# Performance work log

Measured on AMD Instinct MI355X. Metric: run time of the kernel, lower is better.

Reference implementation:

```python
import jax, jax.numpy as jnp
import numpy as np

HEADS = 16

def setup_inputs() -> dict:
    key = jax.random.key(0)
    ks = jax.random.split(key, 5)
    dim = 1024
    x = jax.random.normal(ks[0], (2, 2048, dim), dtype=jnp.float32)
    scale = 1.0 / np.sqrt(dim)
    Wq = jax.random.normal(ks[1], (dim, dim), dtype=jnp.float32) * scale
    Wk = jax.random.normal(ks[2], (dim, dim), dtype=jnp.float32) * scale
    Wv = jax.random.normal(ks[3], (dim, dim), dtype=jnp.float32) * scale
    Wo = jax.random.normal(ks[4], (dim, dim), dtype=jnp.float32) * scale
    return {"x": x, "Wq": Wq, "Wk": Wk, "Wv": Wv, "Wo": Wo}

def reference(x, Wq, Wk, Wv, Wo):
    b, n, dim = x.shape
    h = HEADS
    d = dim // h
    # projections: torch Linear y = x @ W.T (W is [out,in])
    def split_heads(t):
        return t.reshape(b, n, h, d).transpose(0, 2, 1, 3)  # b h n d
    q = split_heads(x @ Wq.T)
    k = split_heads(x @ Wk.T)
    v = split_heads(x @ Wv.T)
    scale = jnp.asarray(d, x.dtype) ** -0.5
    dots = jnp.einsum('bhid,bhjd->bhij', q, k) * scale
    # causal mask: positions j > i masked (triu with diagonal 1 since i == j)
    i_idx = jnp.arange(n)[:, None]
    j_idx = jnp.arange(n)[None, :]
    mask_value = -jnp.finfo(dots.dtype).max
    dots = jnp.where(j_idx > i_idx, mask_value, dots)
    attn = jax.nn.softmax(dots, axis=-1)  # dropout p=0 (eval) is identity
    out = jnp.einsum('bhij,bhjd->bhid', attn, v)
    out = out.transpose(0, 2, 1, 3).reshape(b, n, dim)
    return out @ Wo.T
```

## Files before the change

kernel.cpp:

```cpp
#include <hip/hip_runtime.h>
#include <hip/hip_bf16.h>

#define BATCH 2
#define SEQ   2048
#define DIM   1024
#define HEADS 16
#define DIMH  64
#define BK    32
#define LOG2E 1.44269504088896340736f
#define SM_SHIFT 16.0f

typedef __attribute__((ext_vector_type(8))) short short8;
typedef __attribute__((ext_vector_type(4))) short short4v;
typedef __attribute__((ext_vector_type(4))) float floatx4;

static __device__ __forceinline__ void gload_lds16(const void* g, void* l) {
    __builtin_amdgcn_global_load_lds(
        (const __attribute__((address_space(1))) void*)g,
        (__attribute__((address_space(3))) void*)l, 16, 0, 0);
}

static __device__ __forceinline__ unsigned pk_trunc(float a, float b) {
    return (__float_as_uint(b) & 0xffff0000u) | (__float_as_uint(a) >> 16);
}

__global__ __launch_bounds__(256) void conv_all(
    const float* __restrict__ x,  const float* __restrict__ Wq,
    const float* __restrict__ Wk, const float* __restrict__ Wv,
    const float* __restrict__ Wo,
    __hip_bfloat16* __restrict__ dst, __hip_bfloat16* __restrict__ dwo)
{
    const size_t NX = (size_t)BATCH * SEQ * DIM;
    const size_t NW = (size_t)DIM * DIM;
    size_t i = ((size_t)blockIdx.x * 256 + threadIdx.x) * 4;
    if (i >= NX + 4 * NW) return;
    const float* src; __hip_bfloat16* d;
    if (i < NX) { src = x + i; d = dst + i; }
    else if (i < NX + 3 * NW) {
        size_t j = i - NX;
        int w = (int)(j >> 20);
        src = ((w == 0) ? Wq : (w == 1) ? Wk : Wv) + (j & (NW - 1));
        d = dst + i;
    } else {
        size_t off = i - (NX + 3 * NW);
        src = Wo + off; d = dwo + off;
    }
    floatx4 f = *reinterpret_cast<const floatx4*>(src);
    short4v o;
    #pragma unroll
    for (int e = 0; e < 4; ++e) {
        __hip_bfloat16 t = __float2bfloat16(f[e]);
        o[e] = *reinterpret_cast<short*>(&t);
    }
    *reinterpret_cast<short4v*>(d) = o;
}

__global__ __launch_bounds__(256) void gemm_qkv(
    const __hip_bfloat16* __restrict__ xbf,
    const __hip_bfloat16* __restrict__ wbf,
    __hip_bfloat16* __restrict__ qkv)
{
    __shared__ __align__(16) short As[128 * BK];
    __shared__ __align__(16) short Bs[128 * BK];

    const int tid  = threadIdx.x;
    const int wv   = tid >> 6;
    const int lane = tid & 63;
    const int quad = lane >> 4;
    const int l16  = lane & 15;
    const int wm   = wv >> 1, wn = wv & 1;
    const int m0   = blockIdx.x * 128;
    const int n0   = blockIdx.y * 128;
    const int z    = n0 >> 10;
    __hip_bfloat16* out = qkv + (size_t)z * (BATCH * SEQ * DIM);

    const int srow = tid >> 2;
    const int scol = (tid & 3) * 8;

    floatx4 acc[4][4] = {};

    for (int k0 = 0; k0 < DIM; k0 += BK) {
        __syncthreads();
        #pragma unroll
        for (int i = 0; i < 2; ++i) {
            const __hip_bfloat16* ga = xbf + (size_t)(m0 + srow + i * 64) * DIM + k0 + scol;
            const __hip_bfloat16* gb = wbf + (size_t)(n0 + srow + i * 64) * DIM + k0 + scol;
            gload_lds16(ga, (char*)As + i * 4096 + wv * 1024);
            gload_lds16(gb, (char*)Bs + i * 4096 + wv * 1024);
        }
        __syncthreads();

        short8 af[4], bf[4];
        #pragma unroll
        for (int mt = 0; mt < 4; ++mt)
            af[mt] = *reinterpret_cast<const short8*>(&As[(wm * 64 + mt * 16 + l16) * 32 + quad * 8]);
        #pragma unroll
        for (int nt = 0; nt < 4; ++nt)
            bf[nt] = *reinterpret_cast<const short8*>(&Bs[(wn * 64 + nt * 16 + l16) * 32 + quad * 8]);
        #pragma unroll
        for (int mt = 0; mt < 4; ++mt)
            #pragma unroll
            for (int nt = 0; nt < 4; ++nt)
                acc[mt][nt] = __builtin_amdgcn_mfma_f32_16x16x32_bf16(
                    af[mt], bf[nt], acc[mt][nt], 0, 0, 0);
    }

    const float esc = (z == 0) ? (0.125f * LOG2E) : 1.0f;
    #pragma unroll
    for (int mt = 0; mt < 4; ++mt) {
        #pragma unroll
        for (int nt = 0; nt < 4; ++nt) {
            const int n  = n0 + wn * 64 + nt * 16 + l16;
            const int hh = (n >> 6) & 15, dv = n & 63;
            #pragma unroll
            for (int r = 0; r < 4; ++r) {
                const int m  = m0 + wm * 64 + mt * 16 + quad * 4 + r;
                const int bb = m >> 11, nn = m & (SEQ - 1);
                const float v = acc[mt][nt][r] * esc;
                if (z < 2)
                    out[((size_t)(bb * HEADS + hh) * SEQ + nn) * DIMH + dv] = __float2bfloat16(v);
                else
                    out[((size_t)(bb * HEADS + hh) * DIMH + dv) * SEQ + nn] = __float2bfloat16(v);
            }
        }
    }
}

__global__ __launch_bounds__(256) void gemm_out(
    const __hip_bfloat16* __restrict__ qhs,
    const __hip_bfloat16* __restrict__ W,
    float* __restrict__ C)
{
    __shared__ __align__(16) short As[128 * BK];
    __shared__ __align__(16) short Bs[128 * BK];

    const int tid  = threadIdx.x;
    const int wv   = tid >> 6;
    const int lane = tid & 63;
    const int quad = lane >> 4;
    const int l16  = lane & 15;
    const int wm   = wv >> 1, wn = wv & 1;
    const int m0   = blockIdx.x * 128;
    const int n0   = blockIdx.y * 128;

    const int srow = tid >> 2;
    const int scol = (tid & 3) * 8;

    floatx4 acc[4][4] = {};

    for (int k0 = 0; k0 < DIM; k0 += BK) {
        const int h    = k0 >> 6;
        const int koff = k0 & 63;
        __syncthreads();
        #pragma unroll
        for (int i = 0; i < 2; ++i) {
            const int m  = m0 + srow + i * 64;
            const int bb = m >> 11, nn = m & (SEQ - 1);
            gload_lds16(qhs + ((size_t)(bb * HEADS + h) * SEQ + nn) * DIMH + koff + scol,
                        (char*)As + i * 4096 + wv * 1024);
            gload_lds16(W + (size_t)(n0 + srow + i * 64) * DIM + k0 + scol,
                        (char*)Bs + i * 4096 + wv * 1024);
        }
        __syncthreads();

        short8 af[4], bf[4];
        #pragma unroll
        for (int mt = 0; mt < 4; ++mt)
            af[mt] = *reinterpret_cast<const short8*>(&As[(wm * 64 + mt * 16 + l16) * 32 + quad * 8]);
        #pragma unroll
        for (int nt = 0; nt < 4; ++nt)
            bf[nt] = *reinterpret_cast<const short8*>(&Bs[(wn * 64 + nt * 16 + l16) * 32 + quad * 8]);
        #pragma unroll
        for (int mt = 0; mt < 4; ++mt)
            #pragma unroll
            for (int nt = 0; nt < 4; ++nt)
                acc[mt][nt] = __builtin_amdgcn_mfma_f32_16x16x32_bf16(
                    af[mt], bf[nt], acc[mt][nt], 0, 0, 0);
    }

    #pragma unroll
    for (int mt = 0; mt < 4; ++mt)
        #pragma unroll
        for (int nt = 0; nt < 4; ++nt) {
            const int n = n0 + wn * 64 + nt * 16 + l16;
            #pragma unroll
            for (int r = 0; r < 4; ++r) {
                const int m = m0 + wm * 64 + mt * 16 + quad * 4 + r;
                C[(size_t)m * DIM + n] = acc[mt][nt][r];
            }
        }
}

__global__ __launch_bounds__(128) void attn_causal(
    __hip_bfloat16* __restrict__ qkv)
{
    __shared__ __align__(16) short kt[64 * 64];
    __shared__ __align__(16) short vt[64 * 64];
    __shared__ __align__(16) short pt[2][16 * 72];

    const int id    = blockIdx.x;
    const int combo = id & 31;
    const int p     = id >> 5;
    const int b     = combo >> 4;
    const int h     = combo & 15;
    const int tA = p, tB = 63 - p;
    const int nA = (tA + 2) >> 1;
    const int nB = (tB + 2) >> 1;
    const int total = nA + nB;

    const size_t hoff = (size_t)(b * HEADS + h) * SEQ * DIMH;
    const size_t one  = (size_t)BATCH * SEQ * DIM;
    __hip_bfloat16* qb        = qkv + hoff;
    const __hip_bfloat16* kb  = qkv + one + hoff;
    const __hip_bfloat16* vtg = qkv + 2 * one + hoff;

    const int tid  = threadIdx.x;
    const int wv   = tid >> 6;
    const int lane = tid & 63;
    const int quad = lane >> 4;
    const int l16  = lane & 15;
    const int xr   = l16 & 7;

    const short8 kone8 = {0x3F80, 0x3F80, 0x3F80, 0x3F80,
                          0x3F80, 0x3F80, 0x3F80, 0x3F80};

    int q16 = tA * 32 + wv * 16;
    short8 aq0 = *reinterpret_cast<const short8*>(qb + (size_t)(q16 + l16) * DIMH + quad * 8);
    short8 aq1 = *reinterpret_cast<const short8*>(qb + (size_t)(q16 + l16) * DIMH + 32 + quad * 8);
    floatx4 oacc[4] = {};
    floatx4 lsum = {};

    short8 kreg[4], vreg[4];
    #pragma unroll
    for (int i = 0; i < 4; ++i) {
        const int c = tid + 128 * i;
        const int row = c >> 3, jc = c & 7;
        kreg[i] = *reinterpret_cast<const short8*>(kb + (size_t)row * DIMH + jc * 8);
        vreg[i] = *reinterpret_cast<const short8*>(vtg + (size_t)row * SEQ + jc * 8);
    }

    for (int s = 0; s < total; ++s) {
        const bool lastA = (s == nA - 1);
        const int j0 = ((s < nA) ? s : s - nA) * 64;

        __syncthreads();
        #pragma unroll
        for (int i = 0; i < 4; ++i) {
            const int c = tid + 128 * i;
            const int row = c >> 3, jc = c & 7;
            const int off = row * 64 + ((jc ^ (row & 7)) * 8);
            *reinterpret_cast<short8*>(&kt[off]) = kreg[i];
            *reinterpret_cast<short8*>(&vt[off]) = vreg[i];
        }
        __syncthreads();

        if (s + 1 < total) {
            const int s2 = s + 1;
            const int j1 = ((s2 < nA) ? s2 : s2 - nA) * 64;
            #pragma unroll
            for (int i = 0; i < 4; ++i) {
                const int c = tid + 128 * i;
                const int row = c >> 3, jc = c & 7;
                kreg[i] = *reinterpret_cast<const short8*>(kb + (size_t)(j1 + row) * DIMH + jc * 8);
                vreg[i] = *reinterpret_cast<const short8*>(vtg + (size_t)row * SEQ + j1 + jc * 8);
            }
        }

        floatx4 st[4];
        #pragma unroll
        for (int t = 0; t < 4; ++t) {
            const int rw = t * 16 + l16;
            short8 a0 = *reinterpret_cast<const short8*>(&kt[rw * 64 + (quad ^ xr) * 8]);
            short8 a1 = *reinterpret_cast<const short8*>(&kt[rw * 64 + ((quad + 4) ^ xr) * 8]);
            floatx4 zz = {};
            zz    = __builtin_amdgcn_mfma_f32_16x16x32_bf16(a0, aq0, zz, 0, 0, 0);
            st[t] = __builtin_amdgcn_mfma_f32_16x16x32_bf16(a1, aq1, zz, 0, 0, 0);
        }

        if (j0 + 63 > q16) {
            const int qg = q16 + l16;
            #pragma unroll
            for (int t = 0; t < 4; ++t)
                #pragma unroll
                for (int r = 0; r < 4; ++r) {
                    const int jg = j0 + t * 16 + quad * 4 + r;
                    if (jg > qg) st[t][r] = -3.0e38f;
                }
        }

        #pragma unroll
        for (int t = 0; t < 4; ++t)
            #pragma unroll
            for (int r = 0; r < 4; ++r)
                st[t][r] = __builtin_amdgcn_exp2f(st[t][r] - SM_SHIFT);

        #pragma unroll
        for (int t = 0; t < 4; ++t) {
            *reinterpret_cast<unsigned*>(&pt[wv][l16 * 72 + t * 16 + quad * 4]) =
                pk_trunc(st[t][0], st[t][1]);
            *reinterpret_cast<unsigned*>(&pt[wv][l16 * 72 + t * 16 + quad * 4 + 2]) =
                pk_trunc(st[t][2], st[t][3]);
        }
        short8 p0 = *reinterpret_cast<const short8*>(&pt[wv][l16 * 72 + quad * 8]);
        short8 p1 = *reinterpret_cast<const short8*>(&pt[wv][l16 * 72 + 32 + quad * 8]);

        lsum = __builtin_amdgcn_mfma_f32_16x16x32_bf16(kone8, p0, lsum, 0, 0, 0);
        lsum = __builtin_amdgcn_mfma_f32_16x16x32_bf16(kone8, p1, lsum, 0, 0, 0);

        #pragma unroll
        for (int dt = 0; dt < 4; ++dt) {
            const int rw = dt * 16 + l16;
            short8 v0 = *reinterpret_cast<const short8*>(&vt[rw * 64 + (quad ^ xr) * 8]);
            short8 v1 = *reinterpret_cast<const short8*>(&vt[rw * 64 + ((quad + 4) ^ xr) * 8]);
            oacc[dt] = __builtin_amdgcn_mfma_f32_16x16x32_bf16(v0, p0, oacc[dt], 0, 0, 0);
            oacc[dt] = __builtin_amdgcn_mfma_f32_16x16x32_bf16(v1, p1, oacc[dt], 0, 0, 0);
        }

        if (lastA || s == total - 1) {
            const float rl = 1.0f / lsum[0];
            #pragma unroll
            for (int dt = 0; dt < 4; ++dt)
                #pragma unroll
                for (int r = 0; r < 4; ++r)
                    qb[(size_t)(q16 + l16) * DIMH + dt * 16 + quad * 4 + r] =
                        __float2bfloat16(oacc[dt][r] * rl);
            if (lastA) {
                q16 = tB * 32 + wv * 16;
                aq0 = *reinterpret_cast<const short8*>(qb + (size_t)(q16 + l16) * DIMH + quad * 8);
                aq1 = *reinterpret_cast<const short8*>(qb + (size_t)(q16 + l16) * DIMH + 32 + quad * 8);
                #pragma unroll
                for (int dt = 0; dt < 4; ++dt)
                    #pragma unroll
                    for (int r = 0; r < 4; ++r) oacc[dt][r] = 0.f;
                #pragma unroll
                for (int r = 0; r < 4; ++r) lsum[r] = 0.f;
            }
        }
    }
}


extern "C" void kernel_launch(void* const* d_in, const int* in_sizes, int n_in,
                              void* d_out, int out_size, void* d_ws, size_t ws_size,
                              hipStream_t stream) {
    const float* x  = (const float*)d_in[0];
    const float* Wq = (const float*)d_in[1];
    const float* Wk = (const float*)d_in[2];
    const float* Wv = (const float*)d_in[3];
    const float* Wo = (const float*)d_in[4];

    __hip_bfloat16* qkv  = (__hip_bfloat16*)d_ws;
    __hip_bfloat16* wobf = (__hip_bfloat16*)((char*)d_ws + (size_t)24 * 1024 * 1024);

    __hip_bfloat16* xbf = (__hip_bfloat16*)d_out;
    __hip_bfloat16* wbf = xbf + (size_t)BATCH * SEQ * DIM;

    conv_all  <<<8192, 256, 0, stream>>>(x, Wq, Wk, Wv, Wo, xbf, wobf);
    gemm_qkv  <<<dim3((BATCH * SEQ) / 128, (3 * DIM) / 128), 256, 0, stream>>>(xbf, wbf, qkv);
    attn_causal<<<dim3(1024), 128, 0, stream>>>(qkv);
    gemm_out  <<<dim3((BATCH * SEQ) / 128, DIM / 128), 256, 0, stream>>>(qkv, wobf, (float*)d_out);
}
```

Baseline: 192.1 us.

## Split attention KV tile across wave pairs and reduce partial outputs in LDS

Doubles the attention block size to four waves: each pair of waves shares one 16-row query group and splits each 64-key tile into two 32-key halves. Every wave computes scores, the exponentials and the PV product for its half only, and the partial outputs and row sums are combined through LDS (reusing the K/V tiles) before the normalised output is written. This aims to raise parallelism and latency hiding per block during the serial KV loop. In exchange it adds extra barriers and an LDS reduction at each query-tile boundary.

```diff
diff --git a/kernel.cpp b/kernel.cpp
--- a/kernel.cpp
+++ b/kernel.cpp
@@ -191,7 +191,7 @@
         }
 }
 
-__global__ __launch_bounds__(128) void attn_causal(
+__global__ __launch_bounds__(256) void attn_causal(
     __hip_bfloat16* __restrict__ qkv)
 {
     __shared__ __align__(16) short kt[64 * 64];
@@ -216,6 +216,8 @@
 
     const int tid  = threadIdx.x;
     const int wv   = tid >> 6;
+    const int g    = wv >> 1;
+    const int jh   = wv & 1;
     const int lane = tid & 63;
     const int quad = lane >> 4;
     const int l16  = lane & 15;
@@ -224,16 +226,16 @@
     const short8 kone8 = {0x3F80, 0x3F80, 0x3F80, 0x3F80,
                           0x3F80, 0x3F80, 0x3F80, 0x3F80};
 
-    int q16 = tA * 32 + wv * 16;
+    int q16 = tA * 32 + g * 16;
     short8 aq0 = *reinterpret_cast<const short8*>(qb + (size_t)(q16 + l16) * DIMH + quad * 8);
     short8 aq1 = *reinterpret_cast<const short8*>(qb + (size_t)(q16 + l16) * DIMH + 32 + quad * 8);
     floatx4 oacc[4] = {};
     floatx4 lsum = {};
 
-    short8 kreg[4], vreg[4];
+    short8 kreg[2], vreg[2];
     #pragma unroll
-    for (int i = 0; i < 4; ++i) {
-        const int c = tid + 128 * i;
+    for (int i = 0; i < 2; ++i) {
+        const int c = tid + 256 * i;
         const int row = c >> 3, jc = c & 7;
         kreg[i] = *reinterpret_cast<const short8*>(kb + (size_t)row * DIMH + jc * 8);
         vreg[i] = *reinterpret_cast<const short8*>(vtg + (size_t)row * SEQ + jc * 8);
@@ -245,8 +247,8 @@
 
         __syncthreads();
         #pragma unroll
-        for (int i = 0; i < 4; ++i) {
-            const int c = tid + 128 * i;
+        for (int i = 0; i < 2; ++i) {
+            const int c = tid + 256 * i;
             const int row = c >> 3, jc = c & 7;
             const int off = row * 64 + ((jc ^ (row & 7)) * 8);
             *reinterpret_cast<short8*>(&kt[off]) = kreg[i];
@@ -258,74 +260,88 @@
             const int s2 = s + 1;
             const int j1 = ((s2 < nA) ? s2 : s2 - nA) * 64;
             #pragma unroll
-            for (int i = 0; i < 4; ++i) {
-                const int c = tid + 128 * i;
+            for (int i = 0; i < 2; ++i) {
+                const int c = tid + 256 * i;
                 const int row = c >> 3, jc = c & 7;
                 kreg[i] = *reinterpret_cast<const short8*>(kb + (size_t)(j1 + row) * DIMH + jc * 8);
                 vreg[i] = *reinterpret_cast<const short8*>(vtg + (size_t)row * SEQ + j1 + jc * 8);
             }
         }
 
-        floatx4 st[4];
-        #pragma unroll
-        for (int t = 0; t < 4; ++t) {
+        floatx4 st[2];
+        #pragma unroll
+        for (int tt = 0; tt < 2; ++tt) {
+            const int t  = jh * 2 + tt;
             const int rw = t * 16 + l16;
             short8 a0 = *reinterpret_cast<const short8*>(&kt[rw * 64 + (quad ^ xr) * 8]);
             short8 a1 = *reinterpret_cast<const short8*>(&kt[rw * 64 + ((quad + 4) ^ xr) * 8]);
             floatx4 zz = {};
-            zz    = __builtin_amdgcn_mfma_f32_16x16x32_bf16(a0, aq0, zz, 0, 0, 0);
-            st[t] = __builtin_amdgcn_mfma_f32_16x16x32_bf16(a1, aq1, zz, 0, 0, 0);
+            zz     = __builtin_amdgcn_mfma_f32_16x16x32_bf16(a0, aq0, zz, 0, 0, 0);
+            st[tt] = __builtin_amdgcn_mfma_f32_16x16x32_bf16(a1, aq1, zz, 0, 0, 0);
         }
 
         if (j0 + 63 > q16) {
             const int qg = q16 + l16;
             #pragma unroll
-            for (int t = 0; t < 4; ++t)
+            for (int tt = 0; tt < 2; ++tt)
                 #pragma unroll
                 for (int r = 0; r < 4; ++r) {
-                    const int jg = j0 + t * 16 + quad * 4 + r;
-                    if (jg > qg) st[t][r] = -3.0e38f;
+                    const int jg = j0 + (jh * 2 + tt) * 16 + quad * 4 + r;
+                    if (jg > qg) st[tt][r] = -3.0e38f;
                 }
         }
 
         #pragma unroll
-        for (int t = 0; t < 4; ++t)
+        for (int tt = 0; tt < 2; ++tt)
             #pragma unroll
             for (int r = 0; r < 4; ++r)
-                st[t][r] = __builtin_amdgcn_exp2f(st[t][r] - SM_SHIFT);
-
-        #pragma unroll
-        for (int t = 0; t < 4; ++t) {
-            *reinterpret_cast<unsigned*>(&pt[wv][l16 * 72 + t * 16 + quad * 4]) =
-                pk_trunc(st[t][0], st[t][1]);
-            *reinterpret_cast<unsigned*>(&pt[wv][l16 * 72 + t * 16 + quad * 4 + 2]) =
-                pk_trunc(st[t][2], st[t][3]);
-        }
-        short8 p0 = *reinterpret_cast<const short8*>(&pt[wv][l16 * 72 + quad * 8]);
-        short8 p1 = *reinterpret_cast<const short8*>(&pt[wv][l16 * 72 + 32 + quad * 8]);
-
-        lsum = __builtin_amdgcn_mfma_f32_16x16x32_bf16(kone8, p0, lsum, 0, 0, 0);
-        lsum = __builtin_amdgcn_mfma_f32_16x16x32_bf16(kone8, p1, lsum, 0, 0, 0);
+                st[tt][r] = __builtin_amdgcn_exp2f(st[tt][r] - SM_SHIFT);
+
+        #pragma unroll
+        for (int tt = 0; tt < 2; ++tt) {
+            const int t = jh * 2 + tt;
+            *reinterpret_cast<unsigned*>(&pt[g][l16 * 72 + t * 16 + quad * 4]) =
+                pk_trunc(st[tt][0], st[tt][1]);
+            *reinterpret_cast<unsigned*>(&pt[g][l16 * 72 + t * 16 + quad * 4 + 2]) =
+                pk_trunc(st[tt][2], st[tt][3]);
+        }
+        short8 ph = *reinterpret_cast<const short8*>(&pt[g][l16 * 72 + jh * 32 + quad * 8]);
+
+        lsum = __builtin_amdgcn_mfma_f32_16x16x32_bf16(kone8, ph, lsum, 0, 0, 0);
 
         #pragma unroll
         for (int dt = 0; dt < 4; ++dt) {
             const int rw = dt * 16 + l16;
-            short8 v0 = *reinterpret_cast<const short8*>(&vt[rw * 64 + (quad ^ xr) * 8]);
-            short8 v1 = *reinterpret_cast<const short8*>(&vt[rw * 64 + ((quad + 4) ^ xr) * 8]);
-            oacc[dt] = __builtin_amdgcn_mfma_f32_16x16x32_bf16(v0, p0, oacc[dt], 0, 0, 0);
-            oacc[dt] = __builtin_amdgcn_mfma_f32_16x16x32_bf16(v1, p1, oacc[dt], 0, 0, 0);
+            short8 vh = *reinterpret_cast<const short8*>(&vt[rw * 64 + ((quad + 4 * jh) ^ xr) * 8]);
+            oacc[dt] = __builtin_amdgcn_mfma_f32_16x16x32_bf16(vh, ph, oacc[dt], 0, 0, 0);
         }
 
         if (lastA || s == total - 1) {
-            const float rl = 1.0f / lsum[0];
-            #pragma unroll
-            for (int dt = 0; dt < 4; ++dt)
-                #pragma unroll
-                for (int r = 0; r < 4; ++r)
-                    qb[(size_t)(q16 + l16) * DIMH + dt * 16 + quad * 4 + r] =
-                        __float2bfloat16(oacc[dt][r] * rl);
+            __syncthreads();
+            float* xch = reinterpret_cast<float*>(kt);
+            float* xls = reinterpret_cast<float*>(vt);
+            if (jh == 1) {
+                #pragma unroll
+                for (int dt = 0; dt < 4; ++dt)
+                    #pragma unroll
+                    for (int r = 0; r < 4; ++r)
+                        xch[g * 1024 + (dt * 4 + r) * 64 + lane] = oacc[dt][r];
+                xls[g * 64 + lane] = lsum[0];
+            }
+            __syncthreads();
+            if (jh == 0) {
+                const float rl = 1.0f / (lsum[0] + xls[g * 64 + lane]);
+                #pragma unroll
+                for (int dt = 0; dt < 4; ++dt)
+                    #pragma unroll
+                    for (int r = 0; r < 4; ++r) {
+                        const float ov = oacc[dt][r] + xch[g * 1024 + (dt * 4 + r) * 64 + lane];
+                        qb[(size_t)(q16 + l16) * DIMH + dt * 16 + quad * 4 + r] =
+                            __float2bfloat16(ov * rl);
+                    }
+            }
             if (lastA) {
-                q16 = tB * 32 + wv * 16;
+                q16 = tB * 32 + g * 16;
                 aq0 = *reinterpret_cast<const short8*>(qb + (size_t)(q16 + l16) * DIMH + quad * 8);
                 aq1 = *reinterpret_cast<const short8*>(qb + (size_t)(q16 + l16) * DIMH + 32 + quad * 8);
                 #pragma unroll
@@ -357,6 +373,6 @@
 
     conv_all  <<<8192, 256, 0, stream>>>(x, Wq, Wk, Wv, Wo, xbf, wobf);
     gemm_qkv  <<<dim3((BATCH * SEQ) / 128, (3 * DIM) / 128), 256, 0, stream>>>(xbf, wbf, qkv);
-    attn_causal<<<dim3(1024), 128, 0, stream>>>(qkv);
+    attn_causal<<<dim3(1024), 256, 0, stream>>>(qkv);
     gemm_out  <<<dim3((BATCH * SEQ) / 128, DIM / 128), 256, 0, stream>>>(qkv, wobf, (float*)d_out);
 }
```

Measured after the change: 189.0 us. Within noise of the previous version (-1.6%).
